# Optimization experiments

Measured on AMD Instinct MI355X. Metric: run time of the kernel, lower is better.

## Reference

```python
import jax, jax.numpy as jnp
import numpy as np

N_NEIGHBORS = 16
N_CLASSES = 10

def setup_inputs() -> dict:
    key = jax.random.key(0)
    k1, k2, k3 = jax.random.split(key, 3)
    x = jax.random.normal(k1, (1024, 64), dtype=jnp.float32)
    train_data = jax.random.normal(k2, (100000, 64), dtype=jnp.float32)
    train_labels = jax.random.randint(k3, (100000,), 0, N_CLASSES, dtype=jnp.int64)
    return {"x": x, "train_data": train_data, "train_labels": train_labels}

def reference(x, train_data, train_labels):
    # Pairwise L2 distances [B, N] via the quadratic expansion (same math as cdist p=2)
    x2 = jnp.sum(x * x, axis=-1, keepdims=True)            # [B, 1]
    t2 = jnp.sum(train_data * train_data, axis=-1)          # [N]
    d2 = x2 - 2.0 * (x @ train_data.T) + t2                 # [B, N]
    dist = jnp.sqrt(jnp.maximum(d2, 0.0))
    # k smallest distances
    neg_d, idx = jax.lax.top_k(-dist, N_NEIGHBORS)           # [B, k]
    d = -neg_d
    labels = train_labels[idx]                               # [B, k] gather
    # weights = 'distance': inverse distance, with exact-match rows handled
    w = 1.0 / d
    inf_mask = jnp.isinf(w)
    inf_row = jnp.any(inf_mask, axis=1, keepdims=True)
    w = jnp.where(inf_row, inf_mask.astype(w.dtype), w)
    # scatter_add weighted votes into [B, C]
    B = x.shape[0]
    rows = jnp.arange(B)[:, None]
    proba = jnp.zeros((B, N_CLASSES), dtype=w.dtype).at[rows, labels].add(w)
    s = jnp.sum(proba, axis=1, keepdims=True)
    s = jnp.where(s == 0.0, jnp.float32(1.0), s)
    proba = proba / s
    return jnp.argmax(proba, axis=1), proba
```

## Files before the change

### kernel.cpp

```cpp
#include <hip/hip_runtime.h>
#include <math.h>


constexpr int D        = 64;
constexpr int K        = 16;
constexpr int NCLS     = 10;
constexpr int CHUNKLEN = 1024;
constexpr int NCHUNK   = 98;
constexpr int NPAD     = NCHUNK * CHUNKLEN + 32;
constexpr int NSUB     = 32;
constexpr int SUBLEN   = 256;
constexpr int SLOT     = 16;
constexpr int MSEL     = 48;

typedef __attribute__((ext_vector_type(8))) short bf16x8_t;
typedef __attribute__((ext_vector_type(4))) float f32x4_t;
typedef unsigned short ushort_t;

__device__ __forceinline__ ushort_t f32_to_bf16_rne(float f) {
  unsigned int u = __float_as_uint(f);
  unsigned int r = u + 0x7FFFu + ((u >> 16) & 1u);
  return (ushort_t)(r >> 16);
}

__global__ __launch_bounds__(256) void cvt_train(
    const float* __restrict__ t, ushort_t* __restrict__ tb,
    float* __restrict__ t2, int N)
{
  int gid = blockIdx.x * 256 + threadIdx.x;
  int row = gid >> 2, qt = gid & 3;
  if (row >= NPAD) return;
  ushort_t* dst = tb + (size_t)row * D + qt * 16;
  if (row >= N) {
    uint2 z = make_uint2(0u, 0u);
    #pragma unroll
    for (int i = 0; i < 4; ++i) *reinterpret_cast<uint2*>(dst + i * 4) = z;
    if (qt == 0) t2[row] = INFINITY;
    return;
  }
  const float* src = t + (size_t)row * D + qt * 16;
  float nrm = 0.f;
  #pragma unroll
  for (int i = 0; i < 4; ++i) {
    float4 v = *reinterpret_cast<const float4*>(src + i * 4);
    nrm = fmaf(v.x, v.x, nrm); nrm = fmaf(v.y, v.y, nrm);
    nrm = fmaf(v.z, v.z, nrm); nrm = fmaf(v.w, v.w, nrm);
    uint2 hh = make_uint2(
      (unsigned)f32_to_bf16_rne(v.x) | ((unsigned)f32_to_bf16_rne(v.y) << 16),
      (unsigned)f32_to_bf16_rne(v.z) | ((unsigned)f32_to_bf16_rne(v.w) << 16));
    *reinterpret_cast<uint2*>(dst + i * 4) = hh;
  }
  nrm += __shfl_xor(nrm, 1);
  nrm += __shfl_xor(nrm, 2);
  if (qt == 0) t2[row] = nrm;
}

__global__ __launch_bounds__(256) void cvt_x(
    const float* __restrict__ x, ushort_t* __restrict__ xb, int B)
{
  int gid = blockIdx.x * 256 + threadIdx.x;
  int row = gid >> 2, qt = gid & 3;
  if (row >= B) return;
  const float* src = x + (size_t)row * D + qt * 16;
  ushort_t*    dst = xb + (size_t)row * D + qt * 16;
  #pragma unroll
  for (int i = 0; i < 4; ++i) {
    float4 v = *reinterpret_cast<const float4*>(src + i * 4);
    uint2 hh = make_uint2(
      (unsigned)f32_to_bf16_rne(v.x) | ((unsigned)f32_to_bf16_rne(v.y) << 16),
      (unsigned)f32_to_bf16_rne(v.z) | ((unsigned)f32_to_bf16_rne(v.w) << 16));
    *reinterpret_cast<uint2*>(dst + i * 4) = hh;
  }
}

__global__ __launch_bounds__(256) void knn_sample(
    const ushort_t* __restrict__ tb, const ushort_t* __restrict__ xb,
    const float* __restrict__ t2, float* __restrict__ samp)
{
  const int tid = threadIdx.x;
  const int w = tid >> 6, lane = tid & 63;
  const int lh = lane & 15, lg = lane >> 4;
  const int qb = blockIdx.x, sub = blockIdx.y;
  const int q = qb * 64 + w * 16 + lh;

  const ushort_t* xr = xb + (size_t)q * D + lg * 8;
  bf16x8_t B0 = *reinterpret_cast<const bf16x8_t*>(xr);
  bf16x8_t B1 = *reinterpret_cast<const bf16x8_t*>(xr + 32);

  float Ld[8];
  #pragma unroll
  for (int e = 0; e < 8; ++e) Ld[e] = INFINITY;

  const int pstart = sub * SUBLEN;
  const ushort_t* abase = tb + (size_t)pstart * D + lh * D + lg * 8;
  const float* tbase = t2 + pstart + lg * 4;

  bf16x8_t a0c = *reinterpret_cast<const bf16x8_t*>(abase);
  bf16x8_t a1c = *reinterpret_cast<const bf16x8_t*>(abase + 32);
  float4   tvc = *reinterpret_cast<const float4*>(tbase);

  for (int g = 0; g < SUBLEN / 16; ++g) {
    const ushort_t* anx = abase + (size_t)(g + 1) * 16 * D;
    bf16x8_t a0n = *reinterpret_cast<const bf16x8_t*>(anx);
    bf16x8_t a1n = *reinterpret_cast<const bf16x8_t*>(anx + 32);
    float4   tvn = *reinterpret_cast<const float4*>(tbase + (g + 1) * 16);

    f32x4_t c = {0.f, 0.f, 0.f, 0.f};
    c = __builtin_amdgcn_mfma_f32_16x16x32_bf16(a0c, B0, c, 0, 0, 0);
    c = __builtin_amdgcn_mfma_f32_16x16x32_bf16(a1c, B1, c, 0, 0, 0);
    float tmp0 = fmaf(-2.f, c[0], tvc.x);
    float tmp1 = fmaf(-2.f, c[1], tvc.y);
    float tmp2 = fmaf(-2.f, c[2], tvc.z);
    float tmp3 = fmaf(-2.f, c[3], tvc.w);
    #pragma unroll
    for (int r = 0; r < 4; ++r) {
      float tv = (r == 0) ? tmp0 : (r == 1) ? tmp1 : (r == 2) ? tmp2 : tmp3;
      if (tv < Ld[7]) {
        Ld[7] = tv;
        #pragma unroll
        for (int e = 7; e > 0; --e)
          if (Ld[e] < Ld[e - 1]) { float s = Ld[e]; Ld[e] = Ld[e - 1]; Ld[e - 1] = s; }
      }
    }
    a0c = a0n; a1c = a1n; tvc = tvn;
  }

  float* outp = samp + (size_t)q * (NSUB * 32) + sub * 32 + lg * 8;
  *reinterpret_cast<float4*>(outp)     = make_float4(Ld[0], Ld[1], Ld[2], Ld[3]);
  *reinterpret_cast<float4*>(outp + 4) = make_float4(Ld[4], Ld[5], Ld[6], Ld[7]);
}

__global__ __launch_bounds__(256) void knn_theta(
    const float* __restrict__ samp, float* __restrict__ theta, int B)
{
  const int w = threadIdx.x >> 6, lane = threadIdx.x & 63;
  const int q = blockIdx.x * 4 + w;
  if (q >= B) return;

  const float* s = samp + (size_t)q * (NSUB * 32) + lane * 16;
  float4 p0 = *reinterpret_cast<const float4*>(s);
  float4 p1 = *reinterpret_cast<const float4*>(s + 4);
  float4 p2 = *reinterpret_cast<const float4*>(s + 8);
  float4 p3 = *reinterpret_cast<const float4*>(s + 12);
  float L0[8] = {p0.x, p0.y, p0.z, p0.w, p1.x, p1.y, p1.z, p1.w};
  float L1[8] = {p2.x, p2.y, p2.z, p2.w, p3.x, p3.y, p3.z, p3.w};

  float th = INFINITY;
  for (int r = 0; r < K; ++r) {
    float bd = fminf(L0[0], L1[0]);
    #pragma unroll
    for (int sdx = 0; sdx < 6; ++sdx) {
      float od = __shfl_xor(bd, 32 >> sdx);
      bd = fminf(bd, od);
    }
    if (L0[0] == bd) {
      #pragma unroll
      for (int e = 0; e < 7; ++e) L0[e] = L0[e + 1];
      L0[7] = INFINITY;
    }
    if (L1[0] == bd) {
      #pragma unroll
      for (int e = 0; e < 7; ++e) L1[e] = L1[e + 1];
      L1[7] = INFINITY;
    }
    th = bd;
  }
  if (lane == 0) theta[q] = th;
}

__global__ __launch_bounds__(256) void knn_filter(
    const ushort_t* __restrict__ tb, const ushort_t* __restrict__ xb,
    const float* __restrict__ t2, const float* __restrict__ theta,
    int* __restrict__ cnts, int2* __restrict__ cand2)
{
  __shared__ int  cnt_l[64];
  __shared__ int2 list_p[64][SLOT];

  const int tid = threadIdx.x;
  const int w = tid >> 6, lane = tid & 63;
  const int lh = lane & 15, lg = lane >> 4;
  const int qb = blockIdx.x, ch = blockIdx.y;
  const int q0 = qb * 64;
  const int wp0 = ch * CHUNKLEN + w * (CHUNKLEN / 4);

  if (tid < 64) cnt_l[tid] = 0;
  __syncthreads();

  bf16x8_t Bq0[4], Bq1[4];
  float th[4];
  #pragma unroll
  for (int ct = 0; ct < 4; ++ct) {
    const ushort_t* xr = xb + (size_t)(q0 + ct * 16 + lh) * D + lg * 8;
    Bq0[ct] = *reinterpret_cast<const bf16x8_t*>(xr);
    Bq1[ct] = *reinterpret_cast<const bf16x8_t*>(xr + 32);
    th[ct] = theta[q0 + ct * 16 + lh];
  }

  const ushort_t* abase = tb + (size_t)wp0 * D + lh * D + lg * 8;
  const float* tbase = t2 + wp0 + lg * 4;

  bf16x8_t cA0 = *reinterpret_cast<const bf16x8_t*>(abase);
  bf16x8_t cA1 = *reinterpret_cast<const bf16x8_t*>(abase + 32);
  float4   cTA = *reinterpret_cast<const float4*>(tbase);
  bf16x8_t cB0 = *reinterpret_cast<const bf16x8_t*>(abase + (size_t)16 * D);
  bf16x8_t cB1 = *reinterpret_cast<const bf16x8_t*>(abase + (size_t)16 * D + 32);
  float4   cTB = *reinterpret_cast<const float4*>(tbase + 16);

  #define PROCESS(A0_, A1_, TV_, GIDX_)                                          \
    {                                                                            \
      const int pg = wp0 + (GIDX_) * 16 + lg * 4;                                \
      _Pragma("unroll")                                                          \
      for (int ct = 0; ct < 4; ++ct) {                                           \
        f32x4_t c = {0.f, 0.f, 0.f, 0.f};                                        \
        c = __builtin_amdgcn_mfma_f32_16x16x32_bf16(A0_, Bq0[ct], c, 0, 0, 0);   \
        c = __builtin_amdgcn_mfma_f32_16x16x32_bf16(A1_, Bq1[ct], c, 0, 0, 0);   \
        float tmp0 = fmaf(-2.f, c[0], TV_.x);                                    \
        float tmp1 = fmaf(-2.f, c[1], TV_.y);                                    \
        float tmp2 = fmaf(-2.f, c[2], TV_.z);                                    \
        float tmp3 = fmaf(-2.f, c[3], TV_.w);                                    \
        unsigned m = (tmp0 <= th[ct] ? 1u : 0u) | (tmp1 <= th[ct] ? 2u : 0u)     \
                   | (tmp2 <= th[ct] ? 4u : 0u) | (tmp3 <= th[ct] ? 8u : 0u);    \
        if (m) {                                                                 \
          const int qloc = ct * 16 + lh;                                         \
          int n = __popc(m);                                                     \
          int base = atomicAdd(&cnt_l[qloc], n);                                 \
          while (m) {                                                            \
            int r = __ffs(m) - 1; m &= m - 1;                                    \
            float ts = (r == 0) ? tmp0 : (r == 1) ? tmp1 : (r == 2) ? tmp2 : tmp3;\
            if (base < SLOT)                                                     \
              list_p[qloc][base] = make_int2(pg + r, __float_as_int(ts));        \
            ++base;                                                              \
          }                                                                      \
        }                                                                        \
      }                                                                          \
    }

  for (int g = 0; g < 8; ++g) {
    const ushort_t* an = abase + (size_t)(2 * g + 2) * 16 * D;
    bf16x8_t nA0 = *reinterpret_cast<const bf16x8_t*>(an);
    bf16x8_t nA1 = *reinterpret_cast<const bf16x8_t*>(an + 32);
    float4   nTA = *reinterpret_cast<const float4*>(tbase + (2 * g + 2) * 16);
    bf16x8_t nB0 = *reinterpret_cast<const bf16x8_t*>(an + (size_t)16 * D);
    bf16x8_t nB1 = *reinterpret_cast<const bf16x8_t*>(an + (size_t)16 * D + 32);
    float4   nTB = *reinterpret_cast<const float4*>(tbase + (2 * g + 3) * 16);

    PROCESS(cA0, cA1, cTA, 2 * g);
    PROCESS(cB0, cB1, cTB, 2 * g + 1);

    cA0 = nA0; cA1 = nA1; cTA = nTA;
    cB0 = nB0; cB1 = nB1; cTB = nTB;
  }
  #undef PROCESS

  __syncthreads();
  if (tid < 64) {
    int n = cnt_l[tid]; if (n > SLOT) n = SLOT;
    size_t o = (size_t)(q0 + tid) * NCHUNK + ch;
    cnts[o] = n;
    for (int j = 0; j < n; ++j) cand2[o * SLOT + j] = list_p[tid][j];
  }
}

__global__ __launch_bounds__(256) void knn_vote(
    const float* __restrict__ x, const float* __restrict__ train,
    const float* __restrict__ t2, const int* __restrict__ labels,
    const int* __restrict__ cnts, const int2* __restrict__ cand2,
    float* __restrict__ out, int B, int N)
{
  __shared__ int2  cpair[NCHUNK * SLOT];
  __shared__ float sortd[MSEL];
  __shared__ int   sorti[MSEL];
  __shared__ float xs[D];
  __shared__ int   total_s;
  __shared__ float x2_s;

  const int tid = threadIdx.x;
  const int w = tid >> 6, lane = tid & 63;
  const int q = blockIdx.x;

  if (tid == 0) total_s = 0;
  if (tid < D) xs[tid] = x[(size_t)q * D + tid];
  if (tid < MSEL) { sortd[tid] = INFINITY; sorti[tid] = 0x7fffffff; }
  __syncthreads();

  if (w == 0) {
    float v = xs[lane];
    float s = v * v;
    #pragma unroll
    for (int o = 32; o > 0; o >>= 1) s += __shfl_xor(s, o);
    if (lane == 0) x2_s = s;
  }
  if (tid < NCHUNK) {
    int n = cnts[(size_t)q * NCHUNK + tid];
    int base = atomicAdd(&total_s, n);
    const int2* src = cand2 + ((size_t)q * NCHUNK + tid) * SLOT;
    for (int j = 0; j < n; ++j) cpair[base + j] = src[j];
  }
  __syncthreads();

  const int total = total_s;
  const float x2 = x2_s;

  for (int j = tid; j < total; j += 256) {
    int2 mine = cpair[j];
    float md = __int_as_float(mine.y);
    int   mi = mine.x;
    int rank = 0;
    for (int k = 0; k < total; ++k) {
      int2 o = cpair[k];
      float od = __int_as_float(o.y);
      rank += (od < md || (od == md && o.x < mi)) ? 1 : 0;
    }
    if (rank < MSEL) { sortd[rank] = md; sorti[rank] = mi; }
  }
  __syncthreads();

  if (tid < MSEL) {
    int idx = sorti[tid];
    float d2v = INFINITY;
    if (idx != 0x7fffffff) {
      const float* tr = train + (size_t)idx * D;
      float dot = 0.f;
      #pragma unroll
      for (int i = 0; i < 16; ++i) {
        float4 tv = *reinterpret_cast<const float4*>(tr + i * 4);
        dot = fmaf(xs[i * 4 + 0], tv.x, dot); dot = fmaf(xs[i * 4 + 1], tv.y, dot);
        dot = fmaf(xs[i * 4 + 2], tv.z, dot); dot = fmaf(xs[i * 4 + 3], tv.w, dot);
      }
      d2v = fmaxf(x2 - 2.f * dot + t2[idx], 0.f);
    }
    sortd[tid] = d2v;
  }
  __syncthreads();

  if (w == 0) {
    float vd = (lane < MSEL) ? sortd[lane] : INFINITY;
    int   vi = (lane < MSEL) ? sorti[lane] : 0x7fffffff;
    float myD = INFINITY; int myI = 0;
    for (int r = 0; r < K; ++r) {
      float bd = vd; int bi = vi;
      #pragma unroll
      for (int s = 0; s < 6; ++s) {
        int off = 32 >> s;
        float od = __shfl_xor(bd, off);
        int   oi = __shfl_xor(bi, off);
        if (od < bd || (od == bd && oi < bi)) { bd = od; bi = oi; }
      }
      if (vd == bd && vi == bi) { vd = INFINITY; vi = 0x7fffffff; }
      if (lane == r) { myD = bd; myI = bi; }
    }

    int valid = (lane < K) && (myD < INFINITY) && (myI < N);
    float dist = sqrtf(fmaxf(myD, 0.f));
    int lab = labels[(valid && myI < N) ? myI : 0];
    int isz = (valid && dist == 0.f) ? 1 : 0;
    float wgt = 1.f / dist;

    float accw[NCLS]; float acci[NCLS]; int anyInf = 0;
    #pragma unroll
    for (int c = 0; c < NCLS; ++c) { accw[c] = 0.f; acci[c] = 0.f; }
    for (int r = 0; r < K; ++r) {
      int   vr   = __shfl(valid, r);
      int   labr = __shfl(lab, r);
      float wgtr = __shfl(wgt, r);
      int   iszr = __shfl(isz, r);
      if (vr) {
        anyInf |= iszr;
        #pragma unroll
        for (int c = 0; c < NCLS; ++c) {
          accw[c] += (labr == c) ? wgtr : 0.f;
          acci[c] += (labr == c && iszr) ? 1.f : 0.f;
        }
      }
    }

    if (lane == 0) {
      float proba[NCLS]; float s = 0.f;
      #pragma unroll
      for (int c = 0; c < NCLS; ++c) { proba[c] = anyInf ? acci[c] : accw[c]; s += proba[c]; }
      if (s == 0.f) s = 1.f;
      #pragma unroll
      for (int c = 0; c < NCLS; ++c) proba[c] = proba[c] / s;
      int best = 0; float bv = proba[0];
      #pragma unroll
      for (int c = 1; c < NCLS; ++c) if (proba[c] > bv) { bv = proba[c]; best = c; }
      out[q] = (float)best;
      #pragma unroll
      for (int c = 0; c < NCLS; ++c) out[B + q * NCLS + c] = proba[c];
    }
  }
}

extern "C" void kernel_launch(void* const* d_in, const int* in_sizes, int n_in,
                              void* d_out, int out_size, void* d_ws, size_t ws_size,
                              hipStream_t stream)
{
  const float* x      = (const float*)d_in[0];
  const float* train  = (const float*)d_in[1];
  const int*   labels = (const int*)d_in[2];
  float* out = (float*)d_out;

  const int B = in_sizes[0] / D;
  const int N = in_sizes[2];

  char* ws = (char*)d_ws;
  size_t off = 0;
  ushort_t* train_bf = (ushort_t*)(ws + off); off += (size_t)NPAD * D * 2;
  ushort_t* x_bf     = (ushort_t*)(ws + off); off += (size_t)B * D * 2;
  float*    t2       = (float*)(ws + off);    off += (size_t)NPAD * 4;
  float*    samp     = (float*)(ws + off);    off += (size_t)B * NSUB * 32 * 4;
  float*    theta    = (float*)(ws + off);    off += (size_t)B * 4;
  int*      cnts     = (int*)(ws + off);      off += (size_t)B * NCHUNK * 4;
  int2*     cand2    = (int2*)(ws + off);     off += (size_t)B * NCHUNK * SLOT * 8;

  cvt_train<<<(NPAD * 4 + 255) / 256, 256, 0, stream>>>(train, train_bf, t2, N);
  cvt_x<<<(B * 4 + 255) / 256, 256, 0, stream>>>(x, x_bf, B);
  knn_sample<<<dim3(B / 64, NSUB), 256, 0, stream>>>(train_bf, x_bf, t2, samp);
  knn_theta<<<(B + 3) / 4, 256, 0, stream>>>(samp, theta, B);
  knn_filter<<<dim3(B / 64, NCHUNK), 256, 0, stream>>>(train_bf, x_bf, t2, theta, cnts, cand2);
  knn_vote<<<B, 256, 0, stream>>>(x, train, t2, labels, cnts, cand2, out, B, N);
}
```

Baseline: 114.3 us.

## Fold norm bias into MFMA accumulator, fuse x conversion, reshape sampling pass

Precomputes -0.5*||t||^2 per training row and seeds the MFMA accumulator with it, so the kernels rank by a similarity score (max) rather than computing -2*dot+t2 afterwards. The separate cvt_x kernel is removed and each kernel converts its query rows to bf16 inline. The sampling pass now uses 64 sub-ranges of 128 rows, keeps a top-4 per lane instead of a top-8, and reuses the candidate buffer as scratch for samples. Loads in the filter and sample kernels are batched four groups at a time for deeper prefetch. The aim is to cut a launch, some per-element arithmetic and insertion-sort cost; the risk is a looser threshold that lets more candidates through the filter and more register pressure.

Result: slower. 139.0 us (+21.6%).

```diff
diff --git a/kernel.cpp b/kernel.cpp
--- a/kernel.cpp
+++ b/kernel.cpp
@@ -7,9 +7,9 @@
 constexpr int NCLS     = 10;
 constexpr int CHUNKLEN = 1024;
 constexpr int NCHUNK   = 98;
-constexpr int NPAD     = NCHUNK * CHUNKLEN + 32;
-constexpr int NSUB     = 32;
-constexpr int SUBLEN   = 256;
+constexpr int NPAD     = NCHUNK * CHUNKLEN;
+constexpr int NSUB     = 64;
+constexpr int SUBLEN   = 128;
 constexpr int SLOT     = 16;
 constexpr int MSEL     = 48;
 
@@ -23,9 +23,18 @@
   return (ushort_t)(r >> 16);
 }
 
+__device__ __forceinline__ bf16x8_t pack_bf16x8(float4 a, float4 b) {
+  union { ushort_t u[8]; bf16x8_t v; } r;
+  r.u[0] = f32_to_bf16_rne(a.x); r.u[1] = f32_to_bf16_rne(a.y);
+  r.u[2] = f32_to_bf16_rne(a.z); r.u[3] = f32_to_bf16_rne(a.w);
+  r.u[4] = f32_to_bf16_rne(b.x); r.u[5] = f32_to_bf16_rne(b.y);
+  r.u[6] = f32_to_bf16_rne(b.z); r.u[7] = f32_to_bf16_rne(b.w);
+  return r.v;
+}
+
 __global__ __launch_bounds__(256) void cvt_train(
     const float* __restrict__ t, ushort_t* __restrict__ tb,
-    float* __restrict__ t2, int N)
+    float* __restrict__ t2, float* __restrict__ nt2h, int N)
 {
   int gid = blockIdx.x * 256 + threadIdx.x;
   int row = gid >> 2, qt = gid & 3;
@@ -35,7 +44,7 @@
     uint2 z = make_uint2(0u, 0u);
     #pragma unroll
     for (int i = 0; i < 4; ++i) *reinterpret_cast<uint2*>(dst + i * 4) = z;
-    if (qt == 0) t2[row] = INFINITY;
+    if (qt == 0) { t2[row] = INFINITY; nt2h[row] = -INFINITY; }
     return;
   }
   const float* src = t + (size_t)row * D + qt * 16;
@@ -52,30 +61,12 @@
   }
   nrm += __shfl_xor(nrm, 1);
   nrm += __shfl_xor(nrm, 2);
-  if (qt == 0) t2[row] = nrm;
-}
-
-__global__ __launch_bounds__(256) void cvt_x(
-    const float* __restrict__ x, ushort_t* __restrict__ xb, int B)
-{
-  int gid = blockIdx.x * 256 + threadIdx.x;
-  int row = gid >> 2, qt = gid & 3;
-  if (row >= B) return;
-  const float* src = x + (size_t)row * D + qt * 16;
-  ushort_t*    dst = xb + (size_t)row * D + qt * 16;
-  #pragma unroll
-  for (int i = 0; i < 4; ++i) {
-    float4 v = *reinterpret_cast<const float4*>(src + i * 4);
-    uint2 hh = make_uint2(
-      (unsigned)f32_to_bf16_rne(v.x) | ((unsigned)f32_to_bf16_rne(v.y) << 16),
-      (unsigned)f32_to_bf16_rne(v.z) | ((unsigned)f32_to_bf16_rne(v.w) << 16));
-    *reinterpret_cast<uint2*>(dst + i * 4) = hh;
-  }
+  if (qt == 0) { t2[row] = nrm; nt2h[row] = -0.5f * nrm; }
 }
 
 __global__ __launch_bounds__(256) void knn_sample(
-    const ushort_t* __restrict__ tb, const ushort_t* __restrict__ xb,
-    const float* __restrict__ t2, float* __restrict__ samp)
+    const ushort_t* __restrict__ tb, const float* __restrict__ x,
+    const float* __restrict__ nt2h, float* __restrict__ samp)
 {
   const int tid = threadIdx.x;
   const int w = tid >> 6, lane = tid & 63;
@@ -83,51 +74,70 @@
   const int qb = blockIdx.x, sub = blockIdx.y;
   const int q = qb * 64 + w * 16 + lh;
 
-  const ushort_t* xr = xb + (size_t)q * D + lg * 8;
-  bf16x8_t B0 = *reinterpret_cast<const bf16x8_t*>(xr);
-  bf16x8_t B1 = *reinterpret_cast<const bf16x8_t*>(xr + 32);
-
-  float Ld[8];
-  #pragma unroll
-  for (int e = 0; e < 8; ++e) Ld[e] = INFINITY;
+  const float* xrp = x + (size_t)q * D + lg * 8;
+  bf16x8_t B0 = pack_bf16x8(*reinterpret_cast<const float4*>(xrp),
+                            *reinterpret_cast<const float4*>(xrp + 4));
+  bf16x8_t B1 = pack_bf16x8(*reinterpret_cast<const float4*>(xrp + 32),
+                            *reinterpret_cast<const float4*>(xrp + 36));
+
+  float Ld[4] = {-INFINITY, -INFINITY, -INFINITY, -INFINITY};
 
   const int pstart = sub * SUBLEN;
   const ushort_t* abase = tb + (size_t)pstart * D + lh * D + lg * 8;
-  const float* tbase = t2 + pstart + lg * 4;
-
-  bf16x8_t a0c = *reinterpret_cast<const bf16x8_t*>(abase);
-  bf16x8_t a1c = *reinterpret_cast<const bf16x8_t*>(abase + 32);
-  float4   tvc = *reinterpret_cast<const float4*>(tbase);
-
-  for (int g = 0; g < SUBLEN / 16; ++g) {
-    const ushort_t* anx = abase + (size_t)(g + 1) * 16 * D;
-    bf16x8_t a0n = *reinterpret_cast<const bf16x8_t*>(anx);
-    bf16x8_t a1n = *reinterpret_cast<const bf16x8_t*>(anx + 32);
-    float4   tvn = *reinterpret_cast<const float4*>(tbase + (g + 1) * 16);
-
-    f32x4_t c = {0.f, 0.f, 0.f, 0.f};
-    c = __builtin_amdgcn_mfma_f32_16x16x32_bf16(a0c, B0, c, 0, 0, 0);
-    c = __builtin_amdgcn_mfma_f32_16x16x32_bf16(a1c, B1, c, 0, 0, 0);
-    float tmp0 = fmaf(-2.f, c[0], tvc.x);
-    float tmp1 = fmaf(-2.f, c[1], tvc.y);
-    float tmp2 = fmaf(-2.f, c[2], tvc.z);
-    float tmp3 = fmaf(-2.f, c[3], tvc.w);
+  const float* nbase = nt2h + pstart + lg * 4;
+
+  bf16x8_t A0[4], A1[4]; float4 NH[4];
+  #pragma unroll
+  for (int j = 0; j < 4; ++j) {
+    const ushort_t* ap = abase + (size_t)j * 16 * D;
+    A0[j] = *reinterpret_cast<const bf16x8_t*>(ap);
+    A1[j] = *reinterpret_cast<const bf16x8_t*>(ap + 32);
+    NH[j] = *reinterpret_cast<const float4*>(nbase + j * 16);
+  }
+  bf16x8_t N0[4], N1[4]; float4 NN[4];
+  #pragma unroll
+  for (int j = 0; j < 4; ++j) {
+    const ushort_t* ap = abase + (size_t)(4 + j) * 16 * D;
+    N0[j] = *reinterpret_cast<const bf16x8_t*>(ap);
+    N1[j] = *reinterpret_cast<const bf16x8_t*>(ap + 32);
+    NN[j] = *reinterpret_cast<const float4*>(nbase + (4 + j) * 16);
+  }
+
+  #pragma unroll
+  for (int j = 0; j < 4; ++j) {
+    f32x4_t c = {NH[j].x, NH[j].y, NH[j].z, NH[j].w};
+    c = __builtin_amdgcn_mfma_f32_16x16x32_bf16(A0[j], B0, c, 0, 0, 0);
+    c = __builtin_amdgcn_mfma_f32_16x16x32_bf16(A1[j], B1, c, 0, 0, 0);
     #pragma unroll
     for (int r = 0; r < 4; ++r) {
-      float tv = (r == 0) ? tmp0 : (r == 1) ? tmp1 : (r == 2) ? tmp2 : tmp3;
-      if (tv < Ld[7]) {
-        Ld[7] = tv;
-        #pragma unroll
-        for (int e = 7; e > 0; --e)
-          if (Ld[e] < Ld[e - 1]) { float s = Ld[e]; Ld[e] = Ld[e - 1]; Ld[e - 1] = s; }
-      }
-    }
-    a0c = a0n; a1c = a1n; tvc = tvn;
-  }
-
-  float* outp = samp + (size_t)q * (NSUB * 32) + sub * 32 + lg * 8;
-  *reinterpret_cast<float4*>(outp)     = make_float4(Ld[0], Ld[1], Ld[2], Ld[3]);
-  *reinterpret_cast<float4*>(outp + 4) = make_float4(Ld[4], Ld[5], Ld[6], Ld[7]);
+      float sv = c[r];
+      if (sv > Ld[3]) {
+        Ld[3] = sv;
+        if (Ld[3] > Ld[2]) { float s_ = Ld[3]; Ld[3] = Ld[2]; Ld[2] = s_; }
+        if (Ld[2] > Ld[1]) { float s_ = Ld[2]; Ld[2] = Ld[1]; Ld[1] = s_; }
+        if (Ld[1] > Ld[0]) { float s_ = Ld[1]; Ld[1] = Ld[0]; Ld[0] = s_; }
+      }
+    }
+  }
+  #pragma unroll
+  for (int j = 0; j < 4; ++j) {
+    f32x4_t c = {NN[j].x, NN[j].y, NN[j].z, NN[j].w};
+    c = __builtin_amdgcn_mfma_f32_16x16x32_bf16(N0[j], B0, c, 0, 0, 0);
+    c = __builtin_amdgcn_mfma_f32_16x16x32_bf16(N1[j], B1, c, 0, 0, 0);
+    #pragma unroll
+    for (int r = 0; r < 4; ++r) {
+      float sv = c[r];
+      if (sv > Ld[3]) {
+        Ld[3] = sv;
+        if (Ld[3] > Ld[2]) { float s_ = Ld[3]; Ld[3] = Ld[2]; Ld[2] = s_; }
+        if (Ld[2] > Ld[1]) { float s_ = Ld[2]; Ld[2] = Ld[1]; Ld[1] = s_; }
+        if (Ld[1] > Ld[0]) { float s_ = Ld[1]; Ld[1] = Ld[0]; Ld[0] = s_; }
+      }
+    }
+  }
+
+  float* outp = samp + (size_t)q * (NSUB * 16) + sub * 16 + lg * 4;
+  *reinterpret_cast<float4*>(outp) = make_float4(Ld[0], Ld[1], Ld[2], Ld[3]);
 }
 
 __global__ __launch_bounds__(256) void knn_theta(
@@ -137,40 +147,33 @@
   const int q = blockIdx.x * 4 + w;
   if (q >= B) return;
 
-  const float* s = samp + (size_t)q * (NSUB * 32) + lane * 16;
+  const float* s = samp + (size_t)q * (NSUB * 16) + lane * 16;
   float4 p0 = *reinterpret_cast<const float4*>(s);
   float4 p1 = *reinterpret_cast<const float4*>(s + 4);
   float4 p2 = *reinterpret_cast<const float4*>(s + 8);
   float4 p3 = *reinterpret_cast<const float4*>(s + 12);
-  float L0[8] = {p0.x, p0.y, p0.z, p0.w, p1.x, p1.y, p1.z, p1.w};
-  float L1[8] = {p2.x, p2.y, p2.z, p2.w, p3.x, p3.y, p3.z, p3.w};
-
-  float th = INFINITY;
+  float L0[4] = {p0.x, p0.y, p0.z, p0.w};
+  float L1[4] = {p1.x, p1.y, p1.z, p1.w};
+  float L2[4] = {p2.x, p2.y, p2.z, p2.w};
+  float L3[4] = {p3.x, p3.y, p3.z, p3.w};
+
+  float th = -INFINITY;
   for (int r = 0; r < K; ++r) {
-    float bd = fminf(L0[0], L1[0]);
-    #pragma unroll
-    for (int sdx = 0; sdx < 6; ++sdx) {
-      float od = __shfl_xor(bd, 32 >> sdx);
-      bd = fminf(bd, od);
-    }
-    if (L0[0] == bd) {
-      #pragma unroll
-      for (int e = 0; e < 7; ++e) L0[e] = L0[e + 1];
-      L0[7] = INFINITY;
-    }
-    if (L1[0] == bd) {
-      #pragma unroll
-      for (int e = 0; e < 7; ++e) L1[e] = L1[e + 1];
-      L1[7] = INFINITY;
-    }
+    float bd = fmaxf(fmaxf(L0[0], L1[0]), fmaxf(L2[0], L3[0]));
+    #pragma unroll
+    for (int sdx = 0; sdx < 6; ++sdx) bd = fmaxf(bd, __shfl_xor(bd, 32 >> sdx));
+    if (L0[0] == bd) { L0[0] = L0[1]; L0[1] = L0[2]; L0[2] = L0[3]; L0[3] = -INFINITY; }
+    if (L1[0] == bd) { L1[0] = L1[1]; L1[1] = L1[2]; L1[2] = L1[3]; L1[3] = -INFINITY; }
+    if (L2[0] == bd) { L2[0] = L2[1]; L2[1] = L2[2]; L2[2] = L2[3]; L2[3] = -INFINITY; }
+    if (L3[0] == bd) { L3[0] = L3[1]; L3[1] = L3[2]; L3[2] = L3[3]; L3[3] = -INFINITY; }
     th = bd;
   }
   if (lane == 0) theta[q] = th;
 }
 
 __global__ __launch_bounds__(256) void knn_filter(
-    const ushort_t* __restrict__ tb, const ushort_t* __restrict__ xb,
-    const float* __restrict__ t2, const float* __restrict__ theta,
+    const ushort_t* __restrict__ tb, const float* __restrict__ x,
+    const float* __restrict__ nt2h, const float* __restrict__ theta,
     int* __restrict__ cnts, int2* __restrict__ cand2)
 {
   __shared__ int  cnt_l[64];
@@ -190,65 +193,71 @@
   float th[4];
   #pragma unroll
   for (int ct = 0; ct < 4; ++ct) {
-    const ushort_t* xr = xb + (size_t)(q0 + ct * 16 + lh) * D + lg * 8;
-    Bq0[ct] = *reinterpret_cast<const bf16x8_t*>(xr);
-    Bq1[ct] = *reinterpret_cast<const bf16x8_t*>(xr + 32);
+    const float* xrp = x + (size_t)(q0 + ct * 16 + lh) * D + lg * 8;
+    Bq0[ct] = pack_bf16x8(*reinterpret_cast<const float4*>(xrp),
+                          *reinterpret_cast<const float4*>(xrp + 4));
+    Bq1[ct] = pack_bf16x8(*reinterpret_cast<const float4*>(xrp + 32),
+                          *reinterpret_cast<const float4*>(xrp + 36));
     th[ct] = theta[q0 + ct * 16 + lh];
   }
 
   const ushort_t* abase = tb + (size_t)wp0 * D + lh * D + lg * 8;
-  const float* tbase = t2 + wp0 + lg * 4;
-
-  bf16x8_t cA0 = *reinterpret_cast<const bf16x8_t*>(abase);
-  bf16x8_t cA1 = *reinterpret_cast<const bf16x8_t*>(abase + 32);
-  float4   cTA = *reinterpret_cast<const float4*>(tbase);
-  bf16x8_t cB0 = *reinterpret_cast<const bf16x8_t*>(abase + (size_t)16 * D);
-  bf16x8_t cB1 = *reinterpret_cast<const bf16x8_t*>(abase + (size_t)16 * D + 32);
-  float4   cTB = *reinterpret_cast<const float4*>(tbase + 16);
-
-  #define PROCESS(A0_, A1_, TV_, GIDX_)                                          \
-    {                                                                            \
-      const int pg = wp0 + (GIDX_) * 16 + lg * 4;                                \
-      _Pragma("unroll")                                                          \
-      for (int ct = 0; ct < 4; ++ct) {                                           \
-        f32x4_t c = {0.f, 0.f, 0.f, 0.f};                                        \
-        c = __builtin_amdgcn_mfma_f32_16x16x32_bf16(A0_, Bq0[ct], c, 0, 0, 0);   \
-        c = __builtin_amdgcn_mfma_f32_16x16x32_bf16(A1_, Bq1[ct], c, 0, 0, 0);   \
-        float tmp0 = fmaf(-2.f, c[0], TV_.x);                                    \
-        float tmp1 = fmaf(-2.f, c[1], TV_.y);                                    \
-        float tmp2 = fmaf(-2.f, c[2], TV_.z);                                    \
-        float tmp3 = fmaf(-2.f, c[3], TV_.w);                                    \
-        unsigned m = (tmp0 <= th[ct] ? 1u : 0u) | (tmp1 <= th[ct] ? 2u : 0u)     \
-                   | (tmp2 <= th[ct] ? 4u : 0u) | (tmp3 <= th[ct] ? 8u : 0u);    \
-        if (m) {                                                                 \
-          const int qloc = ct * 16 + lh;                                         \
-          int n = __popc(m);                                                     \
-          int base = atomicAdd(&cnt_l[qloc], n);                                 \
-          while (m) {                                                            \
-            int r = __ffs(m) - 1; m &= m - 1;                                    \
-            float ts = (r == 0) ? tmp0 : (r == 1) ? tmp1 : (r == 2) ? tmp2 : tmp3;\
-            if (base < SLOT)                                                     \
-              list_p[qloc][base] = make_int2(pg + r, __float_as_int(ts));        \
-            ++base;                                                              \
-          }                                                                      \
-        }                                                                        \
-      }                                                                          \
-    }
-
-  for (int g = 0; g < 8; ++g) {
-    const ushort_t* an = abase + (size_t)(2 * g + 2) * 16 * D;
-    bf16x8_t nA0 = *reinterpret_cast<const bf16x8_t*>(an);
-    bf16x8_t nA1 = *reinterpret_cast<const bf16x8_t*>(an + 32);
-    float4   nTA = *reinterpret_cast<const float4*>(tbase + (2 * g + 2) * 16);
-    bf16x8_t nB0 = *reinterpret_cast<const bf16x8_t*>(an + (size_t)16 * D);
-    bf16x8_t nB1 = *reinterpret_cast<const bf16x8_t*>(an + (size_t)16 * D + 32);
-    float4   nTB = *reinterpret_cast<const float4*>(tbase + (2 * g + 3) * 16);
-
-    PROCESS(cA0, cA1, cTA, 2 * g);
-    PROCESS(cB0, cB1, cTB, 2 * g + 1);
-
-    cA0 = nA0; cA1 = nA1; cTA = nTA;
-    cB0 = nB0; cB1 = nB1; cTB = nTB;
+  const float* nbase = nt2h + wp0 + lg * 4;
+
+  bf16x8_t A0[4], A1[4]; float4 NH[4];
+  #pragma unroll
+  for (int j = 0; j < 4; ++j) {
+    const ushort_t* ap = abase + (size_t)j * 16 * D;
+    A0[j] = *reinterpret_cast<const bf16x8_t*>(ap);
+    A1[j] = *reinterpret_cast<const bf16x8_t*>(ap + 32);
+    NH[j] = *reinterpret_cast<const float4*>(nbase + j * 16);
+  }
+
+  #define PROCESS(A0_, A1_, NH_, GIDX_)                                           \
+    {                                                                             \
+      const int pg = wp0 + (GIDX_) * 16 + lg * 4;                                 \
+      _Pragma("unroll")                                                           \
+      for (int ct = 0; ct < 4; ++ct) {                                            \
+        f32x4_t c = {NH_.x, NH_.y, NH_.z, NH_.w};                                 \
+        c = __builtin_amdgcn_mfma_f32_16x16x32_bf16(A0_, Bq0[ct], c, 0, 0, 0);    \
+        c = __builtin_amdgcn_mfma_f32_16x16x32_bf16(A1_, Bq1[ct], c, 0, 0, 0);    \
+        unsigned m = (c[0] >= th[ct] ? 1u : 0u) | (c[1] >= th[ct] ? 2u : 0u)      \
+                   | (c[2] >= th[ct] ? 4u : 0u) | (c[3] >= th[ct] ? 8u : 0u);     \
+        if (m) {                                                                  \
+          const int qloc = ct * 16 + lh;                                          \
+          int n = __popc(m);                                                      \
+          int base = atomicAdd(&cnt_l[qloc], n);                                  \
+          while (m) {                                                             \
+            int r = __ffs(m) - 1; m &= m - 1;                                     \
+            float sv = (r == 0) ? c[0] : (r == 1) ? c[1] : (r == 2) ? c[2] : c[3];\
+            if (base < SLOT)                                                      \
+              list_p[qloc][base] = make_int2(pg + r, __float_as_int(sv));         \
+            ++base;                                                               \
+          }                                                                       \
+        }                                                                         \
+      }                                                                           \
+    }
+
+  for (int it = 0; it < 4; ++it) {
+    bf16x8_t N0[4], N1[4]; float4 NN[4];
+    if (it < 3) {
+      #pragma unroll
+      for (int j = 0; j < 4; ++j) {
+        const int gi = (it + 1) * 4 + j;
+        const ushort_t* ap = abase + (size_t)gi * 16 * D;
+        N0[j] = *reinterpret_cast<const bf16x8_t*>(ap);
+        N1[j] = *reinterpret_cast<const bf16x8_t*>(ap + 32);
+        NN[j] = *reinterpret_cast<const float4*>(nbase + gi * 16);
+      }
+    }
+    PROCESS(A0[0], A1[0], NH[0], it * 4 + 0);
+    PROCESS(A0[1], A1[1], NH[1], it * 4 + 1);
+    PROCESS(A0[2], A1[2], NH[2], it * 4 + 2);
+    PROCESS(A0[3], A1[3], NH[3], it * 4 + 3);
+    if (it < 3) {
+      #pragma unroll
+      for (int j = 0; j < 4; ++j) { A0[j] = N0[j]; A1[j] = N1[j]; NH[j] = NN[j]; }
+    }
   }
   #undef PROCESS
 
@@ -303,15 +312,15 @@
 
   for (int j = tid; j < total; j += 256) {
     int2 mine = cpair[j];
-    float md = __int_as_float(mine.y);
+    float ms = __int_as_float(mine.y);
     int   mi = mine.x;
     int rank = 0;
     for (int k = 0; k < total; ++k) {
       int2 o = cpair[k];
-      float od = __int_as_float(o.y);
-      rank += (od < md || (od == md && o.x < mi)) ? 1 : 0;
-    }
-    if (rank < MSEL) { sortd[rank] = md; sorti[rank] = mi; }
+      float os = __int_as_float(o.y);
+      rank += (os > ms || (os == ms && o.x < mi)) ? 1 : 0;
+    }
+    if (rank < MSEL) { sortd[rank] = ms; sorti[rank] = mi; }
   }
   __syncthreads();
 
@@ -406,17 +415,16 @@
   char* ws = (char*)d_ws;
   size_t off = 0;
   ushort_t* train_bf = (ushort_t*)(ws + off); off += (size_t)NPAD * D * 2;
-  ushort_t* x_bf     = (ushort_t*)(ws + off); off += (size_t)B * D * 2;
   float*    t2       = (float*)(ws + off);    off += (size_t)NPAD * 4;
-  float*    samp     = (float*)(ws + off);    off += (size_t)B * NSUB * 32 * 4;
+  float*    nt2h     = (float*)(ws + off);    off += (size_t)NPAD * 4;
   float*    theta    = (float*)(ws + off);    off += (size_t)B * 4;
   int*      cnts     = (int*)(ws + off);      off += (size_t)B * NCHUNK * 4;
   int2*     cand2    = (int2*)(ws + off);     off += (size_t)B * NCHUNK * SLOT * 8;
-
-  cvt_train<<<(NPAD * 4 + 255) / 256, 256, 0, stream>>>(train, train_bf, t2, N);
-  cvt_x<<<(B * 4 + 255) / 256, 256, 0, stream>>>(x, x_bf, B);
-  knn_sample<<<dim3(B / 64, NSUB), 256, 0, stream>>>(train_bf, x_bf, t2, samp);
+  float*    samp     = (float*)cand2;
+
+  cvt_train<<<(NPAD * 4 + 255) / 256, 256, 0, stream>>>(train, train_bf, t2, nt2h, N);
+  knn_sample<<<dim3(B / 64, NSUB), 256, 0, stream>>>(train_bf, x, nt2h, samp);
   knn_theta<<<(B + 3) / 4, 256, 0, stream>>>(samp, theta, B);
-  knn_filter<<<dim3(B / 64, NCHUNK), 256, 0, stream>>>(train_bf, x_bf, t2, theta, cnts, cand2);
+  knn_filter<<<dim3(B / 64, NCHUNK), 256, 0, stream>>>(train_bf, x, nt2h, theta, cnts, cand2);
   knn_vote<<<B, 256, 0, stream>>>(x, train, t2, labels, cnts, cand2, out, B, N);
 }
```
